# Kernel tuning notes

Measured on AMD Instinct MI355X. Metric: run time of the kernel, lower is better.

Reference implementation:

```python
import jax, jax.numpy as jnp
import numpy as np

H = 4        # heads
C = 128      # out_channels per head (concat=False)
D = 128      # hidden_dim
N = 50000    # nodes
E = 800000   # edges (before self loops)
SLOPE = 0.2  # leaky_relu negative slope (PyG default)


def setup_inputs() -> dict:
    key = jax.random.key(0)
    k0, k1, k2, k3, k4 = jax.random.split(key, 5)
    x = jax.random.normal(k0, (N, D), dtype=jnp.float32)
    edge_index = jax.random.randint(k1, (2, E), 0, N)
    W = jax.random.normal(k2, (D, H * C), dtype=jnp.float32) * (1.0 / np.sqrt(D))
    att_src = jax.random.normal(k3, (H, C), dtype=jnp.float32) * 0.1
    att_dst = jax.random.normal(k4, (H, C), dtype=jnp.float32) * 0.1
    bias = jnp.zeros((C,), dtype=jnp.float32)
    return {"x": x, "edge_index": edge_index, "W": W,
            "att_src": att_src, "att_dst": att_dst, "bias": bias}


def reference(x, edge_index, W, att_src, att_dst, bias):
    n = x.shape[0]
    # add self loops (add_self_loops=True)
    loop = jnp.arange(n, dtype=edge_index.dtype)
    src = jnp.concatenate([edge_index[0], loop])  # message sources
    dst = jnp.concatenate([edge_index[1], loop])  # aggregation targets

    h = (x @ W).reshape(n, H, C)                  # [N, H, C]
    a_src = jnp.einsum('nhc,hc->nh', h, att_src)  # [N, H]
    a_dst = jnp.einsum('nhc,hc->nh', h, att_dst)  # [N, H]

    # per-edge attention logits + leaky relu
    e = a_src[src] + a_dst[dst]                   # [Etot, H]
    e = jnp.where(e >= 0, e, SLOPE * e)

    # scatter-softmax over incoming edges of each dst node
    m = jax.ops.segment_max(e, dst, num_segments=n)      # [N, H]
    p = jnp.exp(e - m[dst])                              # [Etot, H]
    s = jax.ops.segment_sum(p, dst, num_segments=n)      # [N, H]
    alpha = p / s[dst]                                   # [Etot, H]

    # weighted scatter-aggregate of source features
    msg = alpha[:, :, None] * h[src]                     # [Etot, H, C]
    out = jax.ops.segment_sum(msg, dst, num_segments=n)  # [N, H, C]

    # concat=False -> mean over heads, then bias (dropout = identity in eval)
    return out.mean(axis=1) + bias
```

## Files before the change

kernel.cpp:

```cpp
#include <hip/hip_runtime.h>
#include <math.h>

typedef __attribute__((ext_vector_type(8))) short bf16x8;
typedef __attribute__((ext_vector_type(4))) float f32x4;

#define MAXDEG 128

__device__ __forceinline__ float lrelu(float v) { return v >= 0.0f ? v : 0.2f * v; }

__device__ __forceinline__ unsigned short f2bf(float f) {
    unsigned u = __builtin_bit_cast(unsigned, f);
    unsigned r = (u + 0x7fffu + ((u >> 16) & 1u)) >> 16;
    return (unsigned short)r;
}
__device__ __forceinline__ float bflo(unsigned u) { return __builtin_bit_cast(float, u << 16); }
__device__ __forceinline__ float bfhi(unsigned u) { return __builtin_bit_cast(float, u & 0xffff0000u); }
__device__ __forceinline__ unsigned pack2bf(float a, float b) {
    return (unsigned)f2bf(a) | ((unsigned)f2bf(b) << 16);
}

__global__ __launch_bounds__(256) void wa_zero(const float* __restrict__ W,
                                               const float* __restrict__ att_src,
                                               const float* __restrict__ att_dst,
                                               float* __restrict__ Wa,
                                               int* __restrict__ deg, int N) {
    const int t = threadIdx.x;
    if ((int)blockIdx.x < 64) {
        int gid = (int)blockIdx.x * 256 + t;
        int o = gid >> 4, l16 = gid & 15;
        int d = o >> 3, j = o & 7;
        int hd = j & 3;
        const float* att = (j < 4) ? att_src : att_dst;
        const float* wp = &W[d * 512 + hd * 128 + l16 * 8];
        const float* ap = &att[hd * 128 + l16 * 8];
        float4 w0 = *(const float4*)wp, w1 = *(const float4*)(wp + 4);
        float4 a0 = *(const float4*)ap, a1 = *(const float4*)(ap + 4);
        float s = w0.x * a0.x + w0.y * a0.y + w0.z * a0.z + w0.w * a0.w +
                  w1.x * a1.x + w1.y * a1.y + w1.z * a1.z + w1.w * a1.w;
        #pragma unroll
        for (int off = 1; off < 16; off <<= 1) s += __shfl_xor(s, off);
        if (l16 == 0) Wa[o] = s;
    } else {
        int i = ((int)blockIdx.x - 64) * 256 + t;
        if (i < N) deg[i] = 0;
    }
}

__global__ __launch_bounds__(256) void prep(const float* __restrict__ x,
                                            const float* __restrict__ W,
                                            const float* __restrict__ Wa,
                                            const int* __restrict__ esrc,
                                            const int* __restrict__ edst, int E,
                                            unsigned* __restrict__ xb32,
                                            unsigned short* __restrict__ Wt,
                                            float* __restrict__ a_src4,
                                            float* __restrict__ a_dst4,
                                            int* __restrict__ deg,
                                            unsigned short* __restrict__ csr16, int N, int nA) {
    const int t = threadIdx.x;
    if ((int)blockIdx.x < nA) {
        const int wid = t >> 6, l = t & 63;
        float wa0[8], wa1[8];
        {
            const float4* wp = (const float4*)&Wa[(l * 2) * 8];
            float4 a0 = wp[0], a1 = wp[1], b0 = wp[2], b1 = wp[3];
            wa0[0] = a0.x; wa0[1] = a0.y; wa0[2] = a0.z; wa0[3] = a0.w;
            wa0[4] = a1.x; wa0[5] = a1.y; wa0[6] = a1.z; wa0[7] = a1.w;
            wa1[0] = b0.x; wa1[1] = b0.y; wa1[2] = b0.z; wa1[3] = b0.w;
            wa1[4] = b1.x; wa1[5] = b1.y; wa1[6] = b1.z; wa1[7] = b1.w;
        }
        #pragma unroll
        for (int nd = 0; nd < 4; nd++) {
            const int n = (int)blockIdx.x * 16 + wid * 4 + nd;
            if (n >= N) continue;
            float2 xv = *(const float2*)&x[(size_t)n * 128 + l * 2];
            xb32[(size_t)n * 64 + l] = pack2bf(xv.x, xv.y);
            float acc[8];
            #pragma unroll
            for (int j = 0; j < 8; j++) acc[j] = fmaf(xv.x, wa0[j], xv.y * wa1[j]);
            #pragma unroll
            for (int off = 1; off < 64; off <<= 1) {
                #pragma unroll
                for (int j = 0; j < 8; j++) acc[j] += __shfl_xor(acc[j], off);
            }
            if (l == 0) {
                *(float4*)&a_src4[n * 4] = make_float4(acc[0], acc[1], acc[2], acc[3]);
                *(float4*)&a_dst4[n * 4] = make_float4(acc[4], acc[5], acc[6], acc[7]);
            }
        }
    } else if ((int)blockIdx.x < nA + 256) {
        int id = ((int)blockIdx.x - nA) * 256 + t;
        int k = id >> 9, n = id & 511;
        Wt[n * 128 + k] = f2bf(W[k * 512 + n]);
    } else {
        int base = ((int)blockIdx.x - nA - 256) * 1024 + t;
        #pragma unroll
        for (int k = 0; k < 4; k++) {
            int i = base + k * 256;
            if (i < E) {
                int d = edst[i];
                int pos = atomicAdd(&deg[d], 1);
                if (pos < MAXDEG) csr16[(size_t)pos * N + d] = (unsigned short)esrc[i];
            }
        }
    }
}

#define LDA 136

__global__ __launch_bounds__(256, 2) void gemm_mfma(const unsigned short* __restrict__ xb,
                                                    const unsigned short* __restrict__ Wt,
                                                    unsigned short* __restrict__ h2, int N) {
    __shared__ unsigned short As[128 * LDA];
    __shared__ unsigned short Bs[128 * LDA];

    const int brow = blockIdx.x * 128;
    const int bcol = blockIdx.y * 128;
    const int t = threadIdx.x;

    #pragma unroll
    for (int i = 0; i < 8; i++) {
        int idx = t + 256 * i;
        int r = idx >> 4, c = idx & 15;
        uint4 v = make_uint4(0u, 0u, 0u, 0u);
        int row = brow + r;
        if (row < N) v = *(const uint4*)&xb[(size_t)row * 128 + c * 8];
        *(uint4*)&As[r * LDA + c * 8] = v;
    }
    #pragma unroll
    for (int i = 0; i < 8; i++) {
        int idx = t + 256 * i;
        int r = idx >> 4, c = idx & 15;
        uint4 v = *(const uint4*)&Wt[(size_t)(bcol + r) * 128 + c * 8];
        *(uint4*)&Bs[r * LDA + c * 8] = v;
    }
    __syncthreads();

    const int wid = t >> 6, l = t & 63;
    const int wr = wid >> 1, wc = wid & 1;
    const int r = l & 15, g = l >> 4;

    f32x4 zero4 = {0.f, 0.f, 0.f, 0.f};
    f32x4 acc[4][4];
    #pragma unroll
    for (int m = 0; m < 4; m++)
        #pragma unroll
        for (int n = 0; n < 4; n++) acc[m][n] = zero4;

    #pragma unroll
    for (int ks = 0; ks < 4; ks++) {
        bf16x8 a[4], b[4];
        #pragma unroll
        for (int m = 0; m < 4; m++)
            a[m] = *(const bf16x8*)&As[(wr * 64 + m * 16 + r) * LDA + ks * 32 + g * 8];
        #pragma unroll
        for (int n = 0; n < 4; n++)
            b[n] = *(const bf16x8*)&Bs[(wc * 64 + n * 16 + r) * LDA + ks * 32 + g * 8];
        #pragma unroll
        for (int m = 0; m < 4; m++)
            #pragma unroll
            for (int n = 0; n < 4; n++)
                acc[m][n] = __builtin_amdgcn_mfma_f32_16x16x32_bf16(a[m], b[n], acc[m][n], 0, 0, 0);
    }

    __syncthreads();
    unsigned short* Cs = As;
    #pragma unroll
    for (int m = 0; m < 4; m++) {
        #pragma unroll
        for (int n = 0; n < 4; n++) {
            #pragma unroll
            for (int j = 0; j < 4; j++) {
                int row = wr * 64 + m * 16 + g * 4 + j;
                int col = wc * 64 + n * 16 + r;
                Cs[row * LDA + col] = f2bf(acc[m][n][j]);
            }
        }
    }
    __syncthreads();
    #pragma unroll
    for (int i = 0; i < 8; i++) {
        int idx = t + 256 * i;
        int row = idx >> 4, c = idx & 15;
        if (brow + row < N) {
            uint4 v = *(const uint4*)&Cs[row * LDA + c * 8];
            *(uint4*)&h2[(size_t)(brow + row) * 512 + bcol + c * 8] = v;
        }
    }
}

#define ACCUM(p, v)                                                            \
    {                                                                          \
        acc[0] = fmaf(p, bflo(v.x), acc[0]);                                   \
        acc[1] = fmaf(p, bfhi(v.x), acc[1]);                                   \
        acc[2] = fmaf(p, bflo(v.y), acc[2]);                                   \
        acc[3] = fmaf(p, bfhi(v.y), acc[3]);                                   \
        acc[4] = fmaf(p, bflo(v.z), acc[4]);                                   \
        acc[5] = fmaf(p, bfhi(v.z), acc[5]);                                   \
        acc[6] = fmaf(p, bflo(v.w), acc[6]);                                   \
        acc[7] = fmaf(p, bfhi(v.w), acc[7]);                                   \
    }

__global__ __launch_bounds__(256) void aggregate(const unsigned short* __restrict__ h2,
                                                 const float* __restrict__ a_src4,
                                                 const float* __restrict__ a_dst4,
                                                 const int* __restrict__ deg,
                                                 const unsigned short* __restrict__ csr16,
                                                 const float* __restrict__ bias,
                                                 float* __restrict__ out, int N) {
    int wid = (blockIdx.x * 256 + threadIdx.x) >> 6;
    int l = threadIdx.x & 63;
    if (wid >= N) return;
    const int n = wid;
    const int hd = l >> 4;

    const float ad_my = a_dst4[n * 4 + hd];
    float acc[8];
    float ssum;
    {
        float p = __expf(lrelu(a_src4[n * 4 + hd] + ad_my));
        ssum = p;
        uint4 v = *(const uint4*)&h2[(size_t)n * 512 + l * 8];
        acc[0] = p * bflo(v.x); acc[1] = p * bfhi(v.x);
        acc[2] = p * bflo(v.y); acc[3] = p * bfhi(v.y);
        acc[4] = p * bflo(v.z); acc[5] = p * bfhi(v.z);
        acc[6] = p * bflo(v.w); acc[7] = p * bfhi(v.w);
    }

    int dg = deg[n];
    if (dg > MAXDEG) dg = MAXDEG;
    const int nb = dg >> 3;

    int sidx[8];
    if (nb > 0) {
        #pragma unroll
        for (int j = 0; j < 8; j++) sidx[j] = csr16[(size_t)j * N + n];
    }
    for (int b = 0; b < nb; b++) {
        int nsidx[8];
        if (b + 1 < nb) {
            #pragma unroll
            for (int j = 0; j < 8; j++)
                nsidx[j] = csr16[(size_t)((b + 1) * 8 + j) * N + n];
        }
        float lg[8];
        #pragma unroll
        for (int j = 0; j < 8; j++) lg[j] = a_src4[sidx[j] * 4 + hd];
        uint4 hv[8];
        #pragma unroll
        for (int j = 0; j < 8; j++) hv[j] = *(const uint4*)&h2[(size_t)sidx[j] * 512 + l * 8];
        float p[8];
        #pragma unroll
        for (int j = 0; j < 8; j++) {
            p[j] = __expf(lrelu(lg[j] + ad_my));
            ssum += p[j];
        }
        #pragma unroll
        for (int j = 0; j < 8; j++) ACCUM(p[j], hv[j]);
        #pragma unroll
        for (int j = 0; j < 8; j++) sidx[j] = nsidx[j];
    }
    for (int e = nb * 8; e < dg; e++) {
        int s = csr16[(size_t)e * N + n];
        float le = a_src4[s * 4 + hd];
        uint4 v = *(const uint4*)&h2[(size_t)s * 512 + l * 8];
        float p = __expf(lrelu(le + ad_my));
        ssum += p;
        ACCUM(p, v);
    }

    float inv = 1.0f / (4.0f * ssum);
    #pragma unroll
    for (int j = 0; j < 8; j++) acc[j] *= inv;
    #pragma unroll
    for (int off = 16; off < 64; off <<= 1) {
        #pragma unroll
        for (int j = 0; j < 8; j++) acc[j] += __shfl_xor(acc[j], off);
    }
    if (l < 16) {
        const float* bp = &bias[l * 8];
        float4 b0 = *(const float4*)bp;
        float4 b1 = *(const float4*)(bp + 4);
        float* op = &out[(size_t)n * 128 + l * 8];
        *(float4*)op = make_float4(acc[0] + b0.x, acc[1] + b0.y, acc[2] + b0.z, acc[3] + b0.w);
        *(float4*)(op + 4) = make_float4(acc[4] + b1.x, acc[5] + b1.y, acc[6] + b1.z, acc[7] + b1.w);
    }
}

extern "C" void kernel_launch(void* const* d_in, const int* in_sizes, int n_in,
                              void* d_out, int out_size, void* d_ws, size_t ws_size,
                              hipStream_t stream) {
    const float* x = (const float*)d_in[0];
    const int* ei = (const int*)d_in[1];
    const float* W = (const float*)d_in[2];
    const float* att_src = (const float*)d_in[3];
    const float* att_dst = (const float*)d_in[4];
    const float* bias = (const float*)d_in[5];
    float* out = (float*)d_out;

    const int N = in_sizes[0] / 128;
    const int E = in_sizes[1] / 2;
    const int* esrc = ei;
    const int* edst = ei + E;

    char* ws = (char*)d_ws;
    size_t off = 0;
    auto alloc = [&](size_t bytes) {
        void* p = ws + off;
        off = (off + bytes + 511) & ~(size_t)511;
        return p;
    };
    unsigned short* h2 = (unsigned short*)alloc((size_t)N * 512 * 2);
    unsigned short* xb = (unsigned short*)alloc((size_t)N * 128 * 2);
    unsigned short* Wt = (unsigned short*)alloc((size_t)512 * 128 * 2);
    float* Wa = (float*)alloc((size_t)1024 * 4);
    float* a_src4 = (float*)alloc((size_t)N * 16);
    float* a_dst4 = (float*)alloc((size_t)N * 16);
    int* deg = (int*)alloc((size_t)N * 4);
    unsigned short* csr16 = (unsigned short*)alloc((size_t)MAXDEG * N * 2);

    const int nZ = (N + 255) / 256;
    wa_zero<<<64 + nZ, 256, 0, stream>>>(W, att_src, att_dst, Wa, deg, N);

    const int nA = (N + 15) / 16;
    const int nE = (E + 1023) / 1024;
    prep<<<nA + 256 + nE, 256, 0, stream>>>(x, W, Wa, esrc, edst, E, (unsigned*)xb, Wt,
                                            a_src4, a_dst4, deg, csr16, N, nA);

    dim3 gg((N + 127) / 128, 4);
    gemm_mfma<<<gg, 256, 0, stream>>>(xb, Wt, h2, N);

    int nwave_blocks = (N * 64 + 255) / 256;
    aggregate<<<nwave_blocks, 256, 0, stream>>>(h2, a_src4, a_dst4, deg, csr16, bias, out, N);
}
```

Before: 219.9 us.

## Load GEMM fragments from global directly and shrink attention-logit shuffle reduction

The GEMM kernel drops LDS staging of the A and B tiles. Each wave now reads its bf16 MFMA fragments straight from global memory, keeping LDS only for the output tile, and the launch bound rises to 3 blocks per SM. In prep, the 8-value wave reduction now does 3 full shuffle rounds and then selects one value per lane, so only one value goes through the remaining 3 rounds. The CSR-building branch also handles 2048 edges per block instead of 1024. The risks are uncoalesced, cache-dependent fragment reads and unguarded reads past the last row of xb in the final tile.

```diff
diff --git a/kernel.cpp b/kernel.cpp
--- a/kernel.cpp
+++ b/kernel.cpp
@@ -69,6 +69,7 @@
             wa1[0] = b0.x; wa1[1] = b0.y; wa1[2] = b0.z; wa1[3] = b0.w;
             wa1[4] = b1.x; wa1[5] = b1.y; wa1[6] = b1.z; wa1[7] = b1.w;
         }
+        const int sel = l & 7;
         #pragma unroll
         for (int nd = 0; nd < 4; nd++) {
             const int n = (int)blockIdx.x * 16 + wid * 4 + nd;
@@ -79,13 +80,22 @@
             #pragma unroll
             for (int j = 0; j < 8; j++) acc[j] = fmaf(xv.x, wa0[j], xv.y * wa1[j]);
             #pragma unroll
-            for (int off = 1; off < 64; off <<= 1) {
+            for (int off = 1; off < 8; off <<= 1) {
                 #pragma unroll
                 for (int j = 0; j < 8; j++) acc[j] += __shfl_xor(acc[j], off);
             }
-            if (l == 0) {
-                *(float4*)&a_src4[n * 4] = make_float4(acc[0], acc[1], acc[2], acc[3]);
-                *(float4*)&a_dst4[n * 4] = make_float4(acc[4], acc[5], acc[6], acc[7]);
+            float a01 = (sel & 1) ? acc[1] : acc[0];
+            float a23 = (sel & 1) ? acc[3] : acc[2];
+            float a45 = (sel & 1) ? acc[5] : acc[4];
+            float a67 = (sel & 1) ? acc[7] : acc[6];
+            float a03 = (sel & 2) ? a23 : a01;
+            float a47 = (sel & 2) ? a67 : a45;
+            float v = (sel & 4) ? a47 : a03;
+            #pragma unroll
+            for (int off = 8; off < 64; off <<= 1) v += __shfl_xor(v, off);
+            if (l < 8) {
+                if (l < 4) a_src4[n * 4 + l] = v;
+                else       a_dst4[n * 4 + (l - 4)] = v;
             }
         }
     } else if ((int)blockIdx.x < nA + 256) {
@@ -93,9 +103,9 @@
         int k = id >> 9, n = id & 511;
         Wt[n * 128 + k] = f2bf(W[k * 512 + n]);
     } else {
-        int base = ((int)blockIdx.x - nA - 256) * 1024 + t;
-        #pragma unroll
-        for (int k = 0; k < 4; k++) {
+        int base = ((int)blockIdx.x - nA - 256) * 2048 + t;
+        #pragma unroll
+        for (int k = 0; k < 8; k++) {
             int i = base + k * 256;
             if (i < E) {
                 int d = edst[i];
@@ -108,38 +118,27 @@
 
 #define LDA 136
 
-__global__ __launch_bounds__(256, 2) void gemm_mfma(const unsigned short* __restrict__ xb,
+__global__ __launch_bounds__(256, 3) void gemm_mfma(const unsigned short* __restrict__ xb,
                                                     const unsigned short* __restrict__ Wt,
                                                     unsigned short* __restrict__ h2, int N) {
-    __shared__ unsigned short As[128 * LDA];
-    __shared__ unsigned short Bs[128 * LDA];
+    __shared__ unsigned short Cs[128 * LDA];
 
     const int brow = blockIdx.x * 128;
     const int bcol = blockIdx.y * 128;
     const int t = threadIdx.x;
-
-    #pragma unroll
-    for (int i = 0; i < 8; i++) {
-        int idx = t + 256 * i;
-        int r = idx >> 4, c = idx & 15;
-        uint4 v = make_uint4(0u, 0u, 0u, 0u);
-        int row = brow + r;
-        if (row < N) v = *(const uint4*)&xb[(size_t)row * 128 + c * 8];
-        *(uint4*)&As[r * LDA + c * 8] = v;
-    }
-    #pragma unroll
-    for (int i = 0; i < 8; i++) {
-        int idx = t + 256 * i;
-        int r = idx >> 4, c = idx & 15;
-        uint4 v = *(const uint4*)&Wt[(size_t)(bcol + r) * 128 + c * 8];
-        *(uint4*)&Bs[r * LDA + c * 8] = v;
-    }
-    __syncthreads();
-
     const int wid = t >> 6, l = t & 63;
     const int wr = wid >> 1, wc = wid & 1;
     const int r = l & 15, g = l >> 4;
 
+    const unsigned short* ap[4];
+    const unsigned short* bp[4];
+    #pragma unroll
+    for (int m = 0; m < 4; m++)
+        ap[m] = &xb[(size_t)(brow + wr * 64 + m * 16 + r) * 128 + g * 8];
+    #pragma unroll
+    for (int n = 0; n < 4; n++)
+        bp[n] = &Wt[(size_t)(bcol + wc * 64 + n * 16 + r) * 128 + g * 8];
+
     f32x4 zero4 = {0.f, 0.f, 0.f, 0.f};
     f32x4 acc[4][4];
     #pragma unroll
@@ -151,11 +150,9 @@
     for (int ks = 0; ks < 4; ks++) {
         bf16x8 a[4], b[4];
         #pragma unroll
-        for (int m = 0; m < 4; m++)
-            a[m] = *(const bf16x8*)&As[(wr * 64 + m * 16 + r) * LDA + ks * 32 + g * 8];
-        #pragma unroll
-        for (int n = 0; n < 4; n++)
-            b[n] = *(const bf16x8*)&Bs[(wc * 64 + n * 16 + r) * LDA + ks * 32 + g * 8];
+        for (int m = 0; m < 4; m++) a[m] = *(const bf16x8*)(ap[m] + ks * 32);
+        #pragma unroll
+        for (int n = 0; n < 4; n++) b[n] = *(const bf16x8*)(bp[n] + ks * 32);
         #pragma unroll
         for (int m = 0; m < 4; m++)
             #pragma unroll
@@ -163,8 +160,6 @@
                 acc[m][n] = __builtin_amdgcn_mfma_f32_16x16x32_bf16(a[m], b[n], acc[m][n], 0, 0, 0);
     }
 
-    __syncthreads();
-    unsigned short* Cs = As;
     #pragma unroll
     for (int m = 0; m < 4; m++) {
         #pragma unroll
@@ -323,7 +318,7 @@
     wa_zero<<<64 + nZ, 256, 0, stream>>>(W, att_src, att_dst, Wa, deg, N);
 
     const int nA = (N + 15) / 16;
-    const int nE = (E + 1023) / 1024;
+    const int nE = (E + 2047) / 2048;
     prep<<<nA + 256 + nE, 256, 0, stream>>>(x, W, Wa, esrc, edst, E, (unsigned*)xb, Wt,
                                             a_src4, a_dst4, deg, csr16, N, nA);
 
```

Result: no change. 215.9 us (-1.8%).
